# Performance work log

Measured on AMD Instinct MI355X. Metric: run time of the kernel, lower is better.

## Reference

```python
import jax, jax.numpy as jnp
import numpy as np

L, H = 6, 8          # n_layer, n_head
LN_EPS = 1e-5


def _ln(x, g, b):
    mu = jnp.mean(x, axis=-1, keepdims=True)
    var = jnp.mean((x - mu) ** 2, axis=-1, keepdims=True)
    return (x - mu) * jax.lax.rsqrt(var + LN_EPS) * g + b


def setup_inputs() -> dict:
    key = jax.random.key(0)
    B, T, V, D = 2, 2048, 32000, 512
    F = 4 * D
    std = 0.02
    ks = jax.random.split(key, 8)
    idx = jax.random.randint(ks[0], (B, T), 0, V)
    wte = jax.random.normal(ks[1], (V, D), dtype=jnp.float32) * std
    wpe = jax.random.normal(ks[2], (T, D), dtype=jnp.float32) * std
    qkv_w = jax.random.normal(ks[3], (L, D, 3 * D), dtype=jnp.float32) * std
    proj_w = jax.random.normal(ks[4], (L, D, D), dtype=jnp.float32) * std
    fc1_w = jax.random.normal(ks[5], (L, D, F), dtype=jnp.float32) * std
    fc2_w = jax.random.normal(ks[6], (L, F, D), dtype=jnp.float32) * std
    return dict(
        idx=idx, wte=wte, wpe=wpe,
        ln1_g=jnp.ones((L, D), jnp.float32), ln1_b=jnp.zeros((L, D), jnp.float32),
        qkv_w=qkv_w, qkv_b=jnp.zeros((L, 3 * D), jnp.float32),
        proj_w=proj_w, proj_b=jnp.zeros((L, D), jnp.float32),
        ln2_g=jnp.ones((L, D), jnp.float32), ln2_b=jnp.zeros((L, D), jnp.float32),
        fc1_w=fc1_w, fc1_b=jnp.zeros((L, F), jnp.float32),
        fc2_w=fc2_w, fc2_b=jnp.zeros((L, D), jnp.float32),
        lnf_g=jnp.ones((D,), jnp.float32), lnf_b=jnp.zeros((D,), jnp.float32),
    )


def reference(idx, wte, wpe, ln1_g, ln1_b, qkv_w, qkv_b, proj_w, proj_b,
              ln2_g, ln2_b, fc1_w, fc1_b, fc2_w, fc2_b, lnf_g, lnf_b):
    B, T = idx.shape
    D = wte.shape[1]
    hd = D // H
    scale = 1.0 / jnp.sqrt(jnp.asarray(hd, wte.dtype))
    x = wte[idx] + wpe[:T]                      # [B,T,D]
    mask = jnp.tril(jnp.ones((T, T), dtype=bool))

    def block(x, p):
        g1, b1, Wqkv, bqkv, Wp, bp, g2, b2, W1, bf1, W2, bf2 = p
        h = _ln(x, g1, b1)
        qkv = h @ Wqkv + bqkv                   # [B,T,3D]
        q, k, v = jnp.split(qkv, 3, axis=-1)
        q = q.reshape(B, T, H, hd)
        k = k.reshape(B, T, H, hd)
        v = v.reshape(B, T, H, hd)
        att = jnp.einsum('bqhd,bkhd->bhqk', q, k) * scale
        att = jnp.where(mask, att, -jnp.inf)
        att = jax.nn.softmax(att, axis=-1)
        y = jnp.einsum('bhqk,bkhd->bqhd', att, v).reshape(B, T, D)
        x = x + y @ Wp + bp
        h = _ln(x, g2, b2)
        x = x + jax.nn.gelu(h @ W1 + bf1, approximate=False) @ W2 + bf2
        return x, None

    x, _ = jax.lax.scan(block, x, (ln1_g, ln1_b, qkv_w, qkv_b, proj_w, proj_b,
                                   ln2_g, ln2_b, fc1_w, fc1_b, fc2_w, fc2_b))
    x = _ln(x, lnf_g, lnf_b)
    logits = x @ wte.T                          # tied head, [B,T,V]
    return logits
```

## Files before the change

### kernel.cpp

```cpp
#include <hip/hip_runtime.h>
#include <hip/hip_bf16.h>
#include <math.h>

#define BB 2
#define TT 2048
#define DD 512
#define HH 8
#define HD 64
#define FF 2048
#define VV 32000
#define LL 6
#define MM (BB * TT)

typedef unsigned int   u32;
typedef unsigned short u16;
typedef __attribute__((ext_vector_type(8))) short short8;
typedef __attribute__((ext_vector_type(4))) float f32x4;

__device__ __forceinline__ u16 f2bf_bits(float f)
{
    __hip_bfloat16 h = __float2bfloat16(f);
    u16 u;
    __builtin_memcpy(&u, &h, 2);
    return u;
}

__device__ __forceinline__ void gll16(const u16* g, u16* l)
{
    __builtin_amdgcn_global_load_lds(
        (const __attribute__((address_space(1))) u32*)g,
        (__attribute__((address_space(3))) u32*)l,
        16, 0, 0);
}

__device__ __forceinline__ float gelu_exact(float v)
{
    return 0.5f * v * (1.0f + erff(v * 0.70710678118654752440f));
}

__device__ __forceinline__ u16* swp(u16* base, int row, int col)
{
    int off = (row * 128 + col * 2) ^ ((row & 7) << 4);
    return (u16*)((char*)base + off);
}
__device__ __forceinline__ const u16* swpc(const u16* base, int row, int col)
{
    int off = (row * 128 + col * 2) ^ ((row & 7) << 4);
    return (const u16*)((const char*)base + off);
}

__global__ __launch_bounds__(128)
void embed_kernel(const int* __restrict__ idx, const float* __restrict__ wte,
                  const float* __restrict__ wpe, float* __restrict__ x)
{
    int row = blockIdx.x;
    int t = row & (TT - 1);
    int tok = idx[row];
    const float4* wt = (const float4*)(wte + (size_t)tok * DD);
    const float4* wp = (const float4*)(wpe + (size_t)t * DD);
    float4 a = wt[threadIdx.x];
    float4 p = wp[threadIdx.x];
    float4 r;
    r.x = a.x + p.x; r.y = a.y + p.y; r.z = a.z + p.z; r.w = a.w + p.w;
    ((float4*)(x + (size_t)row * DD))[threadIdx.x] = r;
}

__global__ __launch_bounds__(256)
void ln_kernel(const float* __restrict__ x, const float* __restrict__ g,
               const float* __restrict__ b, u16* __restrict__ out)
{
    const int wave = threadIdx.x >> 6, lane = threadIdx.x & 63;
    const int row = blockIdx.x * 4 + wave;
    const float* xr = x + (size_t)row * DD;
    const int c = lane * 4;

    float4 v1 = *(const float4*)(xr + c);
    float4 v2 = *(const float4*)(xr + 256 + c);
    float s  = (v1.x + v1.y) + (v1.z + v1.w) + (v2.x + v2.y) + (v2.z + v2.w);
    float ss = v1.x * v1.x + v1.y * v1.y + v1.z * v1.z + v1.w * v1.w
             + v2.x * v2.x + v2.y * v2.y + v2.z * v2.z + v2.w * v2.w;
    #pragma unroll
    for (int o = 32; o; o >>= 1) {
        s  += __shfl_xor(s, o);
        ss += __shfl_xor(ss, o);
    }
    const float mu  = s * (1.0f / DD);
    const float var = ss * (1.0f / DD) - mu * mu;
    const float rs  = rsqrtf(var + 1e-5f);

    float4 g1 = *(const float4*)(g + c);
    float4 b1 = *(const float4*)(b + c);
    float4 g2 = *(const float4*)(g + 256 + c);
    float4 b2 = *(const float4*)(b + 256 + c);

    u16* orow = out + (size_t)row * DD;
    ushort4 o1, o2;
    o1.x = f2bf_bits((v1.x - mu) * rs * g1.x + b1.x);
    o1.y = f2bf_bits((v1.y - mu) * rs * g1.y + b1.y);
    o1.z = f2bf_bits((v1.z - mu) * rs * g1.z + b1.z);
    o1.w = f2bf_bits((v1.w - mu) * rs * g1.w + b1.w);
    o2.x = f2bf_bits((v2.x - mu) * rs * g2.x + b2.x);
    o2.y = f2bf_bits((v2.y - mu) * rs * g2.y + b2.y);
    o2.z = f2bf_bits((v2.z - mu) * rs * g2.z + b2.z);
    o2.w = f2bf_bits((v2.w - mu) * rs * g2.w + b2.w);
    *(ushort4*)(orow + c)       = o1;
    *(ushort4*)(orow + 256 + c) = o2;
}

__global__ __launch_bounds__(256)
void weight_prep_kernel(const float* __restrict__ qkv_w, const float* __restrict__ proj_w,
                        const float* __restrict__ fc1_w, const float* __restrict__ fc2_w,
                        const float* __restrict__ wte,
                        u16* __restrict__ wqa, u16* __restrict__ wpa,
                        u16* __restrict__ w1a, u16* __restrict__ w2a,
                        u16* __restrict__ wteb)
{
    int id = blockIdx.x;
    if (id >= 18432) {
        int i = (id - 18432) * 256 + threadIdx.x;
        float4 v = ((const float4*)wte)[i];
        ushort4 o;
        o.x = f2bf_bits(v.x); o.y = f2bf_bits(v.y);
        o.z = f2bf_bits(v.z); o.w = f2bf_bits(v.w);
        ((ushort4*)wteb)[i] = o;
        return;
    }
    int l = id / 3072, r = id % 3072;
    const float* in; u16* out; int K, N, tt;
    if (r < 768)       { in = qkv_w + (size_t)l * DD * 3 * DD; out = wqa + (size_t)l * 3 * DD * DD; K = DD; N = 3 * DD; tt = r; }
    else if (r < 1024) { in = proj_w + (size_t)l * DD * DD;    out = wpa + (size_t)l * DD * DD;    K = DD; N = DD;     tt = r - 768; }
    else if (r < 2048) { in = fc1_w + (size_t)l * DD * FF;     out = w1a + (size_t)l * DD * FF;    K = DD; N = FF;     tt = r - 1024; }
    else               { in = fc2_w + (size_t)l * FF * DD;     out = w2a + (size_t)l * FF * DD;    K = FF; N = DD;     tt = r - 2048; }
    int ntx = N >> 5;
    int n0 = (tt % ntx) << 5, k0 = (tt / ntx) << 5;
    __shared__ float tile[32][33];
    int tx = threadIdx.x & 31, ty = threadIdx.x >> 5;
    #pragma unroll
    for (int i = 0; i < 4; ++i)
        tile[ty + i * 8][tx] = in[(size_t)(k0 + ty + i * 8) * N + n0 + tx];
    __syncthreads();
    #pragma unroll
    for (int i = 0; i < 4; ++i)
        out[(size_t)(n0 + ty + i * 8) * K + k0 + tx] = f2bf_bits(tile[tx][ty + i * 8]);
}

template<int BN, bool GELU_ACT, bool RESID, bool OUTBF16, bool QKV_SPLIT,
         bool NMAJOR = false, bool NTSTORE = false>
__global__ __launch_bounds__(256)
void mfma_gemm(const u16* __restrict__ A, const u16* __restrict__ Bt,
               const float* __restrict__ bias, const float* __restrict__ resid,
               void* __restrict__ Cout, u16* __restrict__ Vout,
               int M, int N, int K)
{
    constexpr int NJ = BN / 32;
    __shared__ u16 As[2][128 * 64];
    __shared__ u16 Bs[2][BN * 64];

    const int tid  = threadIdx.x;
    const int lane = tid & 63;
    const int w    = tid >> 6;
    const int wr   = w >> 1, wc = w & 1;

    const int nbx = gridDim.x;
    const int nwg = nbx * gridDim.y;
    int bid = blockIdx.y * nbx + blockIdx.x;
    int swz = (bid & 7) * (nwg >> 3) + (bid >> 3);
    int m0, n0;
    if constexpr (NMAJOR) {
        m0 = (swz & 31) * 128;
        n0 = (swz >> 5) * BN;
    } else {
        m0 = (swz / nbx) * 128;
        n0 = (swz % nbx) * BN;
    }

    const int trow = tid >> 3;
    const int tcol = (tid & 7) * 8;
    const u16* ga = A  + (size_t)(m0 + trow) * K + tcol;
    const u16* gb = Bt + (size_t)(n0 + trow) * K + tcol;

    auto stage = [&](int buf, int k0) {
        u16* la = As[buf] + tid * 8;
        u16* lb = Bs[buf] + tid * 8;
        #pragma unroll
        for (int p = 0; p < 4; ++p)
            gll16(ga + k0 + (size_t)p * 32 * K, la + p * 2048);
        #pragma unroll
        for (int p = 0; p < NJ; ++p)
            gll16(gb + k0 + (size_t)p * 32 * K, lb + p * 2048);
    };

    f32x4 acc[4][NJ] = {};

    const int fr = lane & 15;
    const int fk = (lane >> 4) * 8;

    const int nt = K >> 6;
    stage(0, 0);
    for (int t = 0; t < nt; ++t) {
        asm volatile("s_waitcnt vmcnt(0)" ::: "memory");
        __syncthreads();
        if (t + 1 < nt) stage((t + 1) & 1, (t + 1) << 6);

        const u16* as = As[t & 1];
        const u16* bs = Bs[t & 1];
        #pragma unroll
        for (int ks = 0; ks < 2; ++ks) {
            short8 af[4], bfr[NJ];
            #pragma unroll
            for (int f = 0; f < 4; ++f)
                af[f]  = *(const short8*)&as[(wr * 64 + f * 16 + fr) * 64 + ks * 32 + fk];
            #pragma unroll
            for (int f = 0; f < NJ; ++f)
                bfr[f] = *(const short8*)&bs[(wc * (BN / 2) + f * 16 + fr) * 64 + ks * 32 + fk];
            #pragma unroll
            for (int i = 0; i < 4; ++i)
                #pragma unroll
                for (int j = 0; j < NJ; ++j)
                    acc[i][j] = __builtin_amdgcn_mfma_f32_16x16x32_bf16(
                        af[i], bfr[j], acc[i][j], 0, 0, 0);
        }
    }

    const int c0 = n0 + wc * (BN / 2) + fr;
    const int r0 = m0 + wr * 64 + ((lane >> 4) << 2);
    #pragma unroll
    for (int j = 0; j < NJ; ++j) {
        const int c = c0 + j * 16;
        const float bv = bias ? bias[c] : 0.0f;
        #pragma unroll
        for (int i = 0; i < 4; ++i) {
            const int row0 = r0 + i * 16;
            if constexpr (QKV_SPLIT) {
                if (c < 1024) {
                    #pragma unroll
                    for (int r = 0; r < 4; ++r)
                        ((u16*)Cout)[(size_t)(row0 + r) * 1024 + c] =
                            f2bf_bits(acc[i][j][r] + bv);
                } else {
                    ushort4 o;
                    o.x = f2bf_bits(acc[i][j][0] + bv);
                    o.y = f2bf_bits(acc[i][j][1] + bv);
                    o.z = f2bf_bits(acc[i][j][2] + bv);
                    o.w = f2bf_bits(acc[i][j][3] + bv);
                    const int t0 = row0 & (TT - 1);
                    *(ushort4*)&Vout[(((size_t)(row0 >> 11) * 512 + (c - 1024)) << 11) + t0] = o;
                }
            } else {
                #pragma unroll
                for (int r = 0; r < 4; ++r) {
                    const int row = row0 + r;
                    float v = acc[i][j][r] + bv;
                    if constexpr (GELU_ACT) v = gelu_exact(v);
                    if constexpr (RESID) v += resid[(size_t)row * N + c];
                    if constexpr (OUTBF16) {
                        ((u16*)Cout)[(size_t)row * N + c] = f2bf_bits(v);
                    } else if constexpr (NTSTORE) {
                        __builtin_nontemporal_store(v, &((float*)Cout)[(size_t)row * N + c]);
                    } else {
                        ((float*)Cout)[(size_t)row * N + c] = v;
                    }
                }
            }
        }
    }
}

__global__ __launch_bounds__(256)
void attn_kernel(const u16* __restrict__ qkb, const u16* __restrict__ vtb,
                 u16* __restrict__ y)
{
    const int l = blockIdx.x;
    const int u = l & 255, v = l >> 8;
    const int bh = u & 15;
    const int half = u >> 4;
    const int qt = v ? (16 + half) : (15 - half);
    const int h = bh & (HH - 1);
    const int b = bh >> 3;

    __shared__ alignas(16) u16 Qs[4096];
    __shared__ alignas(16) u16 Ks[2][4096];
    __shared__ alignas(16) u16 Vt[2][4096];
    __shared__ alignas(16) u16 Ps[4096];

    const int tid = threadIdx.x;
    const int lane = tid & 63;
    const int w = tid >> 6;
    const int ln = lane & 15, hi = lane >> 4;
    const int q0 = qt * 64;

    const u16* base  = qkb + (size_t)b * TT * 1024 + h * HD;
    const u16* vbase = vtb + (size_t)(b * 512 + h * HD) * TT;

    const int sr = tid >> 2, sc = (tid & 3) * 16;

    {
        const u16* qrow = base + (size_t)(q0 + sr) * 1024;
        *(short8*)swp(Qs, sr, sc)     = *(const short8*)(qrow + sc);
        *(short8*)swp(Qs, sr, sc + 8) = *(const short8*)(qrow + sc + 8);
    }
    short8 rk0, rk1, rv0, rv1;
    {
        const u16* krow = base + (size_t)sr * 1024 + 512;
        rk0 = *(const short8*)(krow + sc);
        rk1 = *(const short8*)(krow + sc + 8);
        const u16* vrow = vbase + (size_t)sr * TT;
        rv0 = *(const short8*)(vrow + sc);
        rv1 = *(const short8*)(vrow + sc + 8);
    }
    __syncthreads();

    short8 aq0 = *(const short8*)swpc(Qs, w * 16 + ln, hi * 8);
    short8 aq1 = *(const short8*)swpc(Qs, w * 16 + ln, 32 + hi * 8);

    const float SC = 0.18033688011112042f;

    float m[4], lsum[4];
    f32x4 oacc[4] = {};
    #pragma unroll
    for (int r = 0; r < 4; ++r) { m[r] = -INFINITY; lsum[r] = 0.0f; }

    for (int kt = 0; kt <= qt; ++kt) {
        u16* ks = Ks[kt & 1];
        u16* vt = Vt[kt & 1];

        *(short8*)swp(ks, sr, sc)     = rk0;
        *(short8*)swp(ks, sr, sc + 8) = rk1;
        *(short8*)swp(vt, sr, sc)     = rv0;
        *(short8*)swp(vt, sr, sc + 8) = rv1;
        __syncthreads();

        if (kt < qt) {
            const int k0n = (kt + 1) * 64;
            const u16* krow = base + (size_t)(k0n + sr) * 1024 + 512;
            rk0 = *(const short8*)(krow + sc);
            rk1 = *(const short8*)(krow + sc + 8);
            const u16* vrow = vbase + (size_t)sr * TT + k0n;
            rv0 = *(const short8*)(vrow + sc);
            rv1 = *(const short8*)(vrow + sc + 8);
        }

        f32x4 sacc[4] = {};
        __builtin_amdgcn_s_setprio(1);
        #pragma unroll
        for (int j = 0; j < 4; ++j) {
            short8 bk0 = *(const short8*)swpc(ks, j * 16 + ln, hi * 8);
            short8 bk1 = *(const short8*)swpc(ks, j * 16 + ln, 32 + hi * 8);
            sacc[j] = __builtin_amdgcn_mfma_f32_16x16x32_bf16(aq0, bk0, sacc[j], 0, 0, 0);
            sacc[j] = __builtin_amdgcn_mfma_f32_16x16x32_bf16(aq1, bk1, sacc[j], 0, 0, 0);
        }
        __builtin_amdgcn_s_setprio(0);

        const bool diag = (kt == qt);
        #pragma unroll
        for (int r = 0; r < 4; ++r) {
            const int qrow = w * 16 + hi * 4 + r;
            float sv[4];
            #pragma unroll
            for (int j = 0; j < 4; ++j) {
                float s = sacc[j][r] * SC;
                if (diag && (j * 16 + ln > qrow)) s = -INFINITY;
                sv[j] = s;
            }
            float rm = fmaxf(fmaxf(sv[0], sv[1]), fmaxf(sv[2], sv[3]));
            #pragma unroll
            for (int o = 1; o < 16; o <<= 1) rm = fmaxf(rm, __shfl_xor(rm, o));
            float mn = fmaxf(m[r], rm);
            float corr = exp2f(m[r] - mn);
            m[r] = mn;
            float p0 = exp2f(sv[0] - mn);
            float p1 = exp2f(sv[1] - mn);
            float p2 = exp2f(sv[2] - mn);
            float p3 = exp2f(sv[3] - mn);
            *swp(Ps, qrow, ln)      = f2bf_bits(p0);
            *swp(Ps, qrow, 16 + ln) = f2bf_bits(p1);
            *swp(Ps, qrow, 32 + ln) = f2bf_bits(p2);
            *swp(Ps, qrow, 48 + ln) = f2bf_bits(p3);
            lsum[r] = lsum[r] * corr + ((p0 + p1) + (p2 + p3));
            #pragma unroll
            for (int db = 0; db < 4; ++db) oacc[db][r] *= corr;
        }

        short8 ap0 = *(const short8*)swpc(Ps, w * 16 + ln, hi * 8);
        short8 ap1 = *(const short8*)swpc(Ps, w * 16 + ln, 32 + hi * 8);
        __builtin_amdgcn_s_setprio(1);
        #pragma unroll
        for (int db = 0; db < 4; ++db) {
            short8 bv0 = *(const short8*)swpc(vt, db * 16 + ln, hi * 8);
            short8 bv1 = *(const short8*)swpc(vt, db * 16 + ln, 32 + hi * 8);
            oacc[db] = __builtin_amdgcn_mfma_f32_16x16x32_bf16(ap0, bv0, oacc[db], 0, 0, 0);
            oacc[db] = __builtin_amdgcn_mfma_f32_16x16x32_bf16(ap1, bv1, oacc[db], 0, 0, 0);
        }
        __builtin_amdgcn_s_setprio(0);
    }

    #pragma unroll
    for (int r = 0; r < 4; ++r) {
        float lt = lsum[r];
        #pragma unroll
        for (int o = 1; o < 16; o <<= 1) lt += __shfl_xor(lt, o);
        const int q = q0 + w * 16 + hi * 4 + r;
        const float inv = 1.0f / lt;
        u16* yrow = y + (size_t)(b * TT + q) * DD + h * HD;
        #pragma unroll
        for (int db = 0; db < 4; ++db)
            yrow[db * 16 + ln] = f2bf_bits(oacc[db][r] * inv);
    }
}

extern "C" void kernel_launch(void* const* d_in, const int* in_sizes, int n_in,
                              void* d_out, int out_size, void* d_ws, size_t ws_size,
                              hipStream_t stream)
{
    const int*   idx    = (const int*)  d_in[0];
    const float* wte    = (const float*)d_in[1];
    const float* wpe    = (const float*)d_in[2];
    const float* ln1_g  = (const float*)d_in[3];
    const float* ln1_b  = (const float*)d_in[4];
    const float* qkv_w  = (const float*)d_in[5];
    const float* qkv_b  = (const float*)d_in[6];
    const float* proj_w = (const float*)d_in[7];
    const float* proj_b = (const float*)d_in[8];
    const float* ln2_g  = (const float*)d_in[9];
    const float* ln2_b  = (const float*)d_in[10];
    const float* fc1_w  = (const float*)d_in[11];
    const float* fc1_b  = (const float*)d_in[12];
    const float* fc2_w  = (const float*)d_in[13];
    const float* fc2_b  = (const float*)d_in[14];
    const float* lnf_g  = (const float*)d_in[15];
    const float* lnf_b  = (const float*)d_in[16];
    float* out = (float*)d_out;

    char* ws = (char*)d_ws;
    float* x    = (float*)(ws);
    u16*   h    = (u16*)(ws + ((size_t)8  << 20));
    u16*   y    = (u16*)(ws + ((size_t)12 << 20));
    u16*   qkb  = (u16*)(ws + ((size_t)16 << 20));
    u16*   vtb  = (u16*)(ws + ((size_t)24 << 20));
    u16*   wqa  = (u16*)(ws + ((size_t)28 << 20));
    u16*   wpa  = (u16*)(ws + ((size_t)38 << 20));
    u16*   w1a  = (u16*)(ws + ((size_t)42 << 20));
    u16*   w2a  = (u16*)(ws + ((size_t)55 << 20));
    u16*   ffb  = (u16*)(ws + ((size_t)68 << 20));
    u16*   wteb = (u16*)(ws + ((size_t)85 << 20));

    embed_kernel<<<MM, 128, 0, stream>>>(idx, wte, wpe, x);

    weight_prep_kernel<<<18432 + 16000, 256, 0, stream>>>(
        qkv_w, proj_w, fc1_w, fc2_w, wte, wqa, wpa, w1a, w2a, wteb);

    for (int l = 0; l < LL; ++l) {
        ln_kernel<<<MM / 4, 256, 0, stream>>>(x, ln1_g + l * DD, ln1_b + l * DD, h);

        mfma_gemm<64, false, false, true, true><<<dim3(24, 32), 256, 0, stream>>>(
            h, wqa + (size_t)l * 3 * DD * DD, qkv_b + (size_t)l * 3 * DD,
            nullptr, qkb, vtb, MM, 3 * DD, DD);

        attn_kernel<<<512, 256, 0, stream>>>(qkb, vtb, y);

        mfma_gemm<32, false, true, false, false><<<dim3(16, 32), 256, 0, stream>>>(
            y, wpa + (size_t)l * DD * DD, proj_b + (size_t)l * DD,
            x, x, nullptr, MM, DD, DD);

        ln_kernel<<<MM / 4, 256, 0, stream>>>(x, ln2_g + l * DD, ln2_b + l * DD, h);

        mfma_gemm<128, true, false, true, false><<<dim3(16, 32), 256, 0, stream>>>(
            h, w1a + (size_t)l * DD * FF, fc1_b + (size_t)l * FF,
            nullptr, ffb, nullptr, MM, FF, DD);

        mfma_gemm<32, false, true, false, false><<<dim3(16, 32), 256, 0, stream>>>(
            ffb, w2a + (size_t)l * FF * DD, fc2_b + (size_t)l * DD,
            x, x, nullptr, MM, DD, FF);
    }

    ln_kernel<<<MM / 4, 256, 0, stream>>>(x, lnf_g, lnf_b, h);

    mfma_gemm<64, false, false, false, false, true, true><<<dim3(500, 32), 256, 0, stream>>>(
        h, wteb, nullptr, nullptr, out, nullptr, MM, VV, DD);
}
```

Measured before the change: 1.089 ms.

## Split attention along KV into two halves with a separate combine kernel

Each query tile's causal KV range is split into two halves processed by separate blocks, doubling the grid from 512 to 1024 blocks. Each block writes unnormalised fp32 partial outputs plus row max and sum to scratch, and a new combine kernel merges them into the bf16 attention output. Q fragments are now loaded directly from global memory into registers instead of staging through shared memory. This is meant to improve occupancy and load balance across the chip, at the cost of an extra launch and fp32 partial traffic per layer. The scratch space overlaps the FFN buffer, which is free at that point.

After: 1.125 ms. 3.4% more time.

```diff
diff --git a/kernel.cpp b/kernel.cpp
--- a/kernel.cpp
+++ b/kernel.cpp
@@ -268,17 +268,18 @@
 
 __global__ __launch_bounds__(256)
 void attn_kernel(const u16* __restrict__ qkb, const u16* __restrict__ vtb,
-                 u16* __restrict__ y)
-{
-    const int l = blockIdx.x;
-    const int u = l & 255, v = l >> 8;
+                 float* __restrict__ Opart, float2* __restrict__ pml)
+{
+    const int lb = blockIdx.x;
+    const int half_k = lb >> 9;
+    const int pl = lb & 511;
+    const int u = pl & 255, v = pl >> 8;
     const int bh = u & 15;
     const int half = u >> 4;
     const int qt = v ? (16 + half) : (15 - half);
     const int h = bh & (HH - 1);
     const int b = bh >> 3;
 
-    __shared__ alignas(16) u16 Qs[4096];
     __shared__ alignas(16) u16 Ks[2][4096];
     __shared__ alignas(16) u16 Vt[2][4096];
     __shared__ alignas(16) u16 Ps[4096];
@@ -289,29 +290,29 @@
     const int ln = lane & 15, hi = lane >> 4;
     const int q0 = qt * 64;
 
+    const int nkt = qt + 1;
+    const int kmid = (nkt + 1) >> 1;
+    const int kt_begin = half_k ? kmid : 0;
+    const int kt_end   = half_k ? nkt  : kmid;
+
     const u16* base  = qkb + (size_t)b * TT * 1024 + h * HD;
     const u16* vbase = vtb + (size_t)(b * 512 + h * HD) * TT;
 
     const int sr = tid >> 2, sc = (tid & 3) * 16;
 
-    {
-        const u16* qrow = base + (size_t)(q0 + sr) * 1024;
-        *(short8*)swp(Qs, sr, sc)     = *(const short8*)(qrow + sc);
-        *(short8*)swp(Qs, sr, sc + 8) = *(const short8*)(qrow + sc + 8);
-    }
+    const u16* qrow = base + (size_t)(q0 + w * 16 + ln) * 1024;
+    short8 aq0 = *(const short8*)(qrow + hi * 8);
+    short8 aq1 = *(const short8*)(qrow + 32 + hi * 8);
+
     short8 rk0, rk1, rv0, rv1;
     {
-        const u16* krow = base + (size_t)sr * 1024 + 512;
+        const u16* krow = base + (size_t)(kt_begin * 64 + sr) * 1024 + 512;
         rk0 = *(const short8*)(krow + sc);
         rk1 = *(const short8*)(krow + sc + 8);
-        const u16* vrow = vbase + (size_t)sr * TT;
+        const u16* vrow = vbase + (size_t)sr * TT + kt_begin * 64;
         rv0 = *(const short8*)(vrow + sc);
         rv1 = *(const short8*)(vrow + sc + 8);
     }
-    __syncthreads();
-
-    short8 aq0 = *(const short8*)swpc(Qs, w * 16 + ln, hi * 8);
-    short8 aq1 = *(const short8*)swpc(Qs, w * 16 + ln, 32 + hi * 8);
 
     const float SC = 0.18033688011112042f;
 
@@ -320,7 +321,7 @@
     #pragma unroll
     for (int r = 0; r < 4; ++r) { m[r] = -INFINITY; lsum[r] = 0.0f; }
 
-    for (int kt = 0; kt <= qt; ++kt) {
+    for (int kt = kt_begin; kt < kt_end; ++kt) {
         u16* ks = Ks[kt & 1];
         u16* vt = Vt[kt & 1];
 
@@ -330,7 +331,7 @@
         *(short8*)swp(vt, sr, sc + 8) = rv1;
         __syncthreads();
 
-        if (kt < qt) {
+        if (kt + 1 < kt_end) {
             const int k0n = (kt + 1) * 64;
             const u16* krow = base + (size_t)(k0n + sr) * 1024 + 512;
             rk0 = *(const short8*)(krow + sc);
@@ -354,12 +355,12 @@
         const bool diag = (kt == qt);
         #pragma unroll
         for (int r = 0; r < 4; ++r) {
-            const int qrow = w * 16 + hi * 4 + r;
+            const int qr = w * 16 + hi * 4 + r;
             float sv[4];
             #pragma unroll
             for (int j = 0; j < 4; ++j) {
                 float s = sacc[j][r] * SC;
-                if (diag && (j * 16 + ln > qrow)) s = -INFINITY;
+                if (diag && (j * 16 + ln > qr)) s = -INFINITY;
                 sv[j] = s;
             }
             float rm = fmaxf(fmaxf(sv[0], sv[1]), fmaxf(sv[2], sv[3]));
@@ -372,10 +373,10 @@
             float p1 = exp2f(sv[1] - mn);
             float p2 = exp2f(sv[2] - mn);
             float p3 = exp2f(sv[3] - mn);
-            *swp(Ps, qrow, ln)      = f2bf_bits(p0);
-            *swp(Ps, qrow, 16 + ln) = f2bf_bits(p1);
-            *swp(Ps, qrow, 32 + ln) = f2bf_bits(p2);
-            *swp(Ps, qrow, 48 + ln) = f2bf_bits(p3);
+            *swp(Ps, qr, ln)      = f2bf_bits(p0);
+            *swp(Ps, qr, 16 + ln) = f2bf_bits(p1);
+            *swp(Ps, qr, 32 + ln) = f2bf_bits(p2);
+            *swp(Ps, qr, 48 + ln) = f2bf_bits(p3);
             lsum[r] = lsum[r] * corr + ((p0 + p1) + (p2 + p3));
             #pragma unroll
             for (int db = 0; db < 4; ++db) oacc[db][r] *= corr;
@@ -394,18 +395,52 @@
         __builtin_amdgcn_s_setprio(0);
     }
 
+    const size_t pb = ((size_t)pl * 2 + half_k) * 64;
     #pragma unroll
     for (int r = 0; r < 4; ++r) {
         float lt = lsum[r];
         #pragma unroll
         for (int o = 1; o < 16; o <<= 1) lt += __shfl_xor(lt, o);
-        const int q = q0 + w * 16 + hi * 4 + r;
-        const float inv = 1.0f / lt;
-        u16* yrow = y + (size_t)(b * TT + q) * DD + h * HD;
+        const int row = w * 16 + hi * 4 + r;
+        float* obase = Opart + (pb + row) * 64;
         #pragma unroll
         for (int db = 0; db < 4; ++db)
-            yrow[db * 16 + ln] = f2bf_bits(oacc[db][r] * inv);
-    }
+            obase[db * 16 + ln] = oacc[db][r];
+        if (ln == 0) pml[pb + row] = make_float2(m[r], lt);
+    }
+}
+
+__global__ __launch_bounds__(256)
+void attn_combine(const float* __restrict__ Opart, const float2* __restrict__ pml,
+                  u16* __restrict__ y)
+{
+    const int pl = blockIdx.x;
+    const int u = pl & 255, v = pl >> 8;
+    const int bh = u & 15;
+    const int half = u >> 4;
+    const int qt = v ? (16 + half) : (15 - half);
+    const int h = bh & (HH - 1);
+    const int b = bh >> 3;
+
+    const int t = threadIdx.x;
+    const int row = t >> 2, d0 = (t & 3) * 16;
+
+    const size_t p0b = ((size_t)pl * 2 + 0) * 64 + row;
+    const size_t p1b = ((size_t)pl * 2 + 1) * 64 + row;
+    float2 ml0 = pml[p0b];
+    float2 ml1 = pml[p1b];
+    float ms = fmaxf(ml0.x, ml1.x);
+    float w0 = exp2f(ml0.x - ms);
+    float w1 = exp2f(ml1.x - ms);
+    float inv = 1.0f / (ml0.y * w0 + ml1.y * w1);
+
+    const float* O0 = Opart + p0b * 64 + d0;
+    const float* O1 = Opart + p1b * 64 + d0;
+    const int q = qt * 64 + row;
+    u16* yrow = y + (size_t)(b * TT + q) * DD + h * HD + d0;
+    #pragma unroll
+    for (int i = 0; i < 16; ++i)
+        yrow[i] = f2bf_bits((O0[i] * w0 + O1[i] * w1) * inv);
 }
 
 extern "C" void kernel_launch(void* const* d_in, const int* in_sizes, int n_in,
@@ -441,7 +476,10 @@
     u16*   wpa  = (u16*)(ws + ((size_t)38 << 20));
     u16*   w1a  = (u16*)(ws + ((size_t)42 << 20));
     u16*   w2a  = (u16*)(ws + ((size_t)55 << 20));
-    u16*   ffb  = (u16*)(ws + ((size_t)68 << 20));
+    char*  scr  = ws + ((size_t)68 << 20);
+    float* Opart= (float*)scr;
+    float2* pml = (float2*)(scr + ((size_t)16 << 20));
+    u16*   ffb  = (u16*)scr;
     u16*   wteb = (u16*)(ws + ((size_t)85 << 20));
 
     embed_kernel<<<MM, 128, 0, stream>>>(idx, wte, wpe, x);
@@ -456,7 +494,8 @@
             h, wqa + (size_t)l * 3 * DD * DD, qkv_b + (size_t)l * 3 * DD,
             nullptr, qkb, vtb, MM, 3 * DD, DD);
 
-        attn_kernel<<<512, 256, 0, stream>>>(qkb, vtb, y);
+        attn_kernel<<<1024, 256, 0, stream>>>(qkb, vtb, Opart, pml);
+        attn_combine<<<512, 256, 0, stream>>>(Opart, pml, y);
 
         mfma_gemm<32, false, true, false, false><<<dim3(16, 32), 256, 0, stream>>>(
             y, wpa + (size_t)l * DD * DD, proj_b + (size_t)l * DD,
```
